# Optimization experiments

Hardware: AMD Instinct MI355X
Metric: run time of the kernel (lower is better)

## Reference

```python
import jax, jax.numpy as jnp
import numpy as np

NEG_SLOPE = 0.2  # PyG GATv2Conv default negative_slope
G = 128          # number of graphs in the batch


def _gatv2(x, src, dst, n, Wl, bl, Wr, br, att, bias, H, C):
    # x: [N, in]; src/dst: [E] (self-loops already appended)
    xl = (x @ Wl + bl).reshape(n, H, C)   # lin_l -> used for source nodes
    xr = (x @ Wr + br).reshape(n, H, C)   # lin_r -> used for target nodes
    e = jax.nn.leaky_relu(xl[src] + xr[dst], NEG_SLOPE)      # [E,H,C]
    logit = jnp.einsum('ehc,hc->eh', e, att)                 # [E,H]
    # softmax over edges grouped by destination node
    m = jax.ops.segment_max(logit, dst, num_segments=n)      # [N,H]
    p = jnp.exp(logit - m[dst])
    denom = jax.ops.segment_sum(p, dst, num_segments=n)
    alpha = p / denom[dst]                                   # [E,H]
    out = jax.ops.segment_sum(xl[src] * alpha[..., None], dst, num_segments=n)
    return out.reshape(n, H * C) + bias                      # concat heads + bias


def setup_inputs() -> dict:
    key = jax.random.key(0)
    ks = jax.random.split(key, 32)
    N, E, V, EMB = 30000, 480000, 10000, 16
    s = 0.1
    d = {
        'emb':  jax.random.normal(ks[0], (V, EMB)) * s,
        'Wl0':  jax.random.normal(ks[1], (16, 96)) * s,
        'bl0':  jax.random.normal(ks[2], (96,)) * s,
        'Wr0':  jax.random.normal(ks[3], (16, 96)) * s,
        'br0':  jax.random.normal(ks[4], (96,)) * s,
        'att0': jax.random.normal(ks[5], (3, 32)) * s,
        'bo0':  jax.random.normal(ks[6], (96,)) * s,
        'Wl1':  jax.random.normal(ks[7], (96, 192)) * s,
        'bl1':  jax.random.normal(ks[8], (192,)) * s,
        'Wr1':  jax.random.normal(ks[9], (96, 192)) * s,
        'br1':  jax.random.normal(ks[10], (192,)) * s,
        'att1': jax.random.normal(ks[11], (2, 96)) * s,
        'bo1':  jax.random.normal(ks[12], (192,)) * s,
        'Wl2':  jax.random.normal(ks[13], (192, 64)) * s,
        'bl2':  jax.random.normal(ks[14], (64,)) * s,
        'Wr2':  jax.random.normal(ks[15], (192, 64)) * s,
        'br2':  jax.random.normal(ks[16], (64,)) * s,
        'att2': jax.random.normal(ks[17], (1, 64)) * s,
        'bo2':  jax.random.normal(ks[18], (64,)) * s,
        'Wc1':  jax.random.normal(ks[19], (69, 32)) * s,
        'bc1':  jax.random.normal(ks[20], (32,)) * s,
        'Wc2':  jax.random.normal(ks[21], (32, 2)) * s,
        'bc2':  jax.random.normal(ks[22], (2,)) * s,
        'demographics': jax.random.normal(ks[23], (G, 5)),
        'node_ids': jax.random.randint(ks[24], (N,), 0, V),
        'edge_index': jax.random.randint(ks[25], (2, E), 0, N),
        'batch': jnp.sort(jax.random.randint(ks[26], (N,), 0, G)),
    }
    return d


def reference(emb, Wl0, bl0, Wr0, br0, att0, bo0,
              Wl1, bl1, Wr1, br1, att1, bo1,
              Wl2, bl2, Wr2, br2, att2, bo2,
              Wc1, bc1, Wc2, bc2, demographics,
              node_ids, edge_index, batch):
    N = node_ids.shape[0]
    x = emb[node_ids]                                  # node embedding lookup
    loops = jnp.arange(N)
    src = jnp.concatenate([edge_index[0], loops])      # PyG add_self_loops=True
    dst = jnp.concatenate([edge_index[1], loops])
    x = _gatv2(x, src, dst, N, Wl0, bl0, Wr0, br0, att0, bo0, 3, 32)
    x = _gatv2(x, src, dst, N, Wl1, bl1, Wr1, br1, att1, bo1, 2, 96)
    x = _gatv2(x, src, dst, N, Wl2, bl2, Wr2, br2, att2, bo2, 1, 64)
    # global mean pool over graphs
    counts = jax.ops.segment_sum(jnp.ones((N,), x.dtype), batch, num_segments=G)
    g = jax.ops.segment_sum(x, batch, num_segments=G) / jnp.maximum(counts, 1.0)[:, None]
    h = jnp.concatenate([g, demographics], axis=1)     # [G, 64+5]
    h = jax.nn.relu(h @ Wc1 + bc1)                     # dropout is identity at eval
    return h @ Wc2 + bc2                               # out_dim=2 -> no squeeze
```

## Files before the change

kernel.cpp:

```cpp
#include <hip/hip_runtime.h>
#include <hip/hip_bf16.h>

typedef __hip_bfloat16 bf16;
typedef __attribute__((ext_vector_type(8))) short short8;
typedef __attribute__((ext_vector_type(4))) float f32x4;

static __device__ __forceinline__ float b2f(bf16 v){ return __bfloat162float(v); }
static __device__ __forceinline__ float blo(unsigned u){ return __uint_as_float(u<<16); }
static __device__ __forceinline__ float bhi(unsigned u){ return __uint_as_float(u & 0xffff0000u); }
static __device__ __forceinline__ int clampi(int v, int lo, int hi){
  return v < lo ? lo : (v > hi ? hi : v);
}
static __device__ __forceinline__ unsigned pack2(float lo, float hi){
  bf16 a = __float2bfloat16(lo), b = __float2bfloat16(hi);
  unsigned short ua, ub;
  __builtin_memcpy(&ua,&a,2); __builtin_memcpy(&ub,&b,2);
  return (unsigned)ua | ((unsigned)ub<<16);
}
static __device__ __forceinline__ float fexp2(float x){ return __builtin_exp2f(x); }

template<int CTRL>
static __device__ __forceinline__ float dppadd(float v){
  int s = __builtin_amdgcn_update_dpp(0, __float_as_int(v), CTRL, 0xf, 0xf, false);
  return v + __int_as_float(s);
}
static __device__ __forceinline__ float red16(float v){
  v = dppadd<0x121>(v);
  v = dppadd<0x122>(v);
  v = dppadd<0x124>(v);
  v = dppadd<0x128>(v);
  return v;
}

constexpr int Nn = 30000;
constexpr int E0 = 480000;
constexpr int EP = E0 + Nn;
constexpr int Gg = 128;
constexpr int Vv = 10000;
constexpr int CAP = 64;
constexpr float L2E = 1.4426950408889634f;

__global__ void k_flag(float* __restrict__ out, float v){
  int t = blockIdx.x*blockDim.x + threadIdx.x;
  if (t < Gg*2) out[t] = v;
}

__global__ void k_prep(const float* __restrict__ emb, const int* __restrict__ ids,
                       bf16* __restrict__ x, int* __restrict__ cursor,
                       const float* __restrict__ W0l, const float* __restrict__ W0r,
                       const float* __restrict__ W1l, const float* __restrict__ W1r,
                       const float* __restrict__ W2l, const float* __restrict__ W2r,
                       bf16* __restrict__ B0l, bf16* __restrict__ B0r,
                       bf16* __restrict__ B1l, bf16* __restrict__ B1r,
                       bf16* __restrict__ B2l, bf16* __restrict__ B2r){
  int t = blockIdx.x*blockDim.x + threadIdx.x;
  if (t < Nn) cursor[t] = 0;
  if (t < 67584){
    const float* W; bf16* B; int K, F, KS, i;
    if      (t <  3072){ i = t;       W = W0l; B = B0l; K=16;  F=96;  KS=1; }
    else if (t <  6144){ i = t-3072;  W = W0r; B = B0r; K=16;  F=96;  KS=1; }
    else if (t < 24576){ i = t-6144;  W = W1l; B = B1l; K=96;  F=192; KS=3; }
    else if (t < 43008){ i = t-24576; W = W1r; B = B1r; K=96;  F=192; KS=3; }
    else if (t < 55296){ i = t-43008; W = W2l; B = B2l; K=192; F=64;  KS=6; }
    else               { i = t-55296; W = W2r; B = B2r; K=192; F=64;  KS=6; }
    int f = i >> 3, j = i & 7;
    int ot   = f / (KS*64);
    int rem  = f % (KS*64);
    int ks   = rem >> 6;
    int lane = rem & 63;
    int l16  = lane & 15, quad = lane >> 4;
    int o = ot*16 + l16;
    int k = ks*32 + quad*8 + j;
    float v = (k < K) ? W[k*F + o] : 0.f;
    B[i] = __float2bfloat16(v);
  }
  if (t < Nn*16){
    int n = t >> 4, c = t & 15;
    int id = clampi(ids[n], 0, Vv-1);
    x[t] = __float2bfloat16(emb[id*16 + c]);
  }
}

template<int K, int Kp, int Fout>
static __device__ __forceinline__
void linB_body(int bid, const bf16* __restrict__ x,
               const bf16* __restrict__ Wbl, const float* __restrict__ bl,
               const bf16* __restrict__ Wbr, const float* __restrict__ br,
               bf16* __restrict__ yl, bf16* __restrict__ yr){
  constexpr int OT = Fout/16, KS = Kp/32;
  constexpr int FR = OT*KS*64;
  __shared__ uint4 sB[FR];
  constexpr int MT = Nn/16;
  int wid = threadIdx.x >> 6, lane = threadIdx.x & 63;
  int grp = bid*4 + wid;
  int l16 = lane & 15, quad = lane >> 4;
  bool havework = (grp < MT);

  short8 a[KS];
  if (havework){
    const bf16* arow = x + (size_t)(grp*16 + l16)*K;
    #pragma unroll
    for (int ks=0; ks<KS; ks++){
      int k0 = ks*32 + quad*8;
      if (K == Kp || k0 < K) a[ks] = *(const short8*)(arow + k0);
      else                   a[ks] = short8{0,0,0,0,0,0,0,0};
    }
  }
  #pragma unroll
  for (int side=0; side<2; side++){
    const bf16*  Wb   = side ? Wbr : Wbl;
    const float* bias = side ? br  : bl;
    bf16*        y    = side ? yr  : yl;
    const uint4* srcp = (const uint4*)Wb;
    for (int idx = threadIdx.x; idx < FR; idx += 256) sB[idx] = srcp[idx];
    __syncthreads();
    if (havework){
      #pragma unroll
      for (int ot=0; ot<OT; ot++){
        f32x4 acc = {0.f,0.f,0.f,0.f};
        #pragma unroll
        for (int ks=0; ks<KS; ks++){
          short8 b = *(const short8*)&sB[(ot*KS + ks)*64 + lane];
          acc = __builtin_amdgcn_mfma_f32_16x16x32_bf16(a[ks], b, acc, 0, 0, 0);
        }
        int o0 = ot*16;
        float bo_ = bias[o0 + l16];
        #pragma unroll
        for (int r=0;r<4;r++){
          int m = grp*16 + quad*4 + r;
          y[(size_t)m*Fout + o0 + l16] = __float2bfloat16(acc[r] + bo_);
        }
      }
    }
    __syncthreads();
  }
}

template<int K, int Kp, int Fout>
__global__ __launch_bounds__(256) void k_linB(const bf16* __restrict__ x,
               const bf16* __restrict__ Wbl, const float* __restrict__ bl,
               const bf16* __restrict__ Wbr, const float* __restrict__ br,
               bf16* __restrict__ yl, bf16* __restrict__ yr){
  linB_body<K,Kp,Fout>(blockIdx.x, x, Wbl, bl, Wbr, br, yl, yr);
}

constexpr int CBcnt = (EP + 255) / 256;
__global__ __launch_bounds__(256) void k_fillin0(const int* __restrict__ ei,
               int* __restrict__ cursor, int* __restrict__ bucket,
               const bf16* __restrict__ x,
               const bf16* __restrict__ Wbl, const float* __restrict__ bl,
               const bf16* __restrict__ Wbr, const float* __restrict__ br,
               bf16* __restrict__ yl, bf16* __restrict__ yr){
  if ((int)blockIdx.x < CBcnt){
    int e = blockIdx.x*256 + threadIdx.x;
    if (e < EP){
      int src = (e < E0) ? clampi(ei[e],      0, Nn-1) : (e - E0);
      int dst = (e < E0) ? clampi(ei[E0 + e], 0, Nn-1) : (e - E0);
      int pos = atomicAdd(&cursor[dst], 1);
      if (pos < CAP) bucket[dst*CAP + pos] = src;
    }
    return;
  }
  linB_body<16,32,96>(blockIdx.x - CBcnt, x, Wbl, bl, Wbr, br, yl, yr);
}


template<int UN, bool MASK>
static __device__ __forceinline__
void idx0(const int* __restrict__ eb, int i, int r1, int g, unsigned off[UN]){
  #pragma unroll
  for (int u=0;u<UN;u++){
    int iu = i + 4*u + g;
    int ii = MASK ? ((iu<r1)? iu : (r1-1)) : iu;
    off[u] = (unsigned)eb[ii] * 96u;
  }
}

template<int UN, bool MASK>
static __device__ __forceinline__
void body0(const bf16* __restrict__ xl0, const unsigned off[UN],
           int i, int r1, int g,
           const float xr2[3][2], const float a06[3][2], const float a04[3][2],
           float acc[3][2], float ds[3]){
  unsigned xw[UN][3];
  #pragma unroll
  for (int u=0;u<UN;u++){
    xw[u][0] = *(const unsigned*)(xl0 + off[u]);
    xw[u][1] = *(const unsigned*)(xl0 + off[u] + 32);
    xw[u][2] = *(const unsigned*)(xl0 + off[u] + 64);
  }
  #pragma unroll
  for (int u=0;u<UN;u++){
    float wm = MASK ? (((i + 4*u + g) < r1) ? 1.f : 0.f) : 1.f;
    #pragma unroll
    for (int h=0;h<3;h++){
      float c0 = blo(xw[u][h]), c1 = bhi(xw[u][h]);
      float z0 = c0 + xr2[h][0], z1 = c1 + xr2[h][1];
      float ts = a06[h][0]*z0;
      ts = fmaf(a04[h][0], __builtin_fabsf(z0), ts);
      ts = fmaf(a06[h][1], z1, ts);
      ts = fmaf(a04[h][1], __builtin_fabsf(z1), ts);
      float hs = red16(ts);
      float p = fexp2(hs);
      if (MASK) p *= wm;
      acc[h][0] += p*c0; acc[h][1] += p*c1; ds[h] += p;
    }
  }
}

__global__ void k_fused0w(const bf16* __restrict__ xl, const bf16* __restrict__ xr,
                          const int* __restrict__ bucket, const int* __restrict__ cursor,
                          const float* __restrict__ att, const float* __restrict__ bo,
                          bf16* __restrict__ y){
  int n = blockIdx.x*(blockDim.x>>6) + (threadIdx.x>>6);
  if (n >= Nn) return;
  int lane = threadIdx.x & 63;
  int g = lane >> 4, l16 = lane & 15, c2 = 2*l16;
  const bf16* xl0 = xl + c2;
  const int* eb = bucket + n*CAP;
  int r1 = cursor[n]; if (r1 > CAP) r1 = CAP;
  float xr2[3][2], a06[3][2], a04[3][2];
  #pragma unroll
  for (int h=0;h<3;h++){
    unsigned wv = *(const unsigned*)(xr + (size_t)n*96 + h*32 + c2);
    xr2[h][0]=blo(wv); xr2[h][1]=bhi(wv);
    float2 av = *(const float2*)(att + h*32 + c2);
    a06[h][0]=0.6f*L2E*av.x; a04[h][0]=0.4f*L2E*av.x;
    a06[h][1]=0.6f*L2E*av.y; a04[h][1]=0.4f*L2E*av.y;
  }
  float acc[3][2] = {{0.f,0.f},{0.f,0.f},{0.f,0.f}};
  float ds[3] = {0.f,0.f,0.f};
  int i = 0;
  int nw = r1 >> 4;
  if (nw > 0){
    unsigned offA[4], offB[4];
    idx0<4,false>(eb, i, r1, g, offA);
    for (int k=0; k<nw-1; k++){
      idx0<4,false>(eb, i+16, r1, g, offB);
      body0<4,false>(xl0, offA, i, r1, g, xr2, a06, a04, acc, ds);
      #pragma unroll
      for (int u=0;u<4;u++) offA[u] = offB[u];
      i += 16;
    }
    body0<4,false>(xl0, offA, i, r1, g, xr2, a06, a04, acc, ds);
    i += 16;
  }
  int rem = r1 - i;
  if (rem > 0){
    unsigned offT[4];
    if (rem > 8){
      idx0<4,true>(eb, i, r1, g, offT);
      body0<4,true>(xl0, offT, i, r1, g, xr2, a06, a04, acc, ds);
    } else if (rem > 4){
      idx0<2,true>(eb, i, r1, g, offT);
      body0<2,true>(xl0, offT, i, r1, g, xr2, a06, a04, acc, ds);
    } else {
      idx0<1,true>(eb, i, r1, g, offT);
      body0<1,true>(xl0, offT, i, r1, g, xr2, a06, a04, acc, ds);
    }
  }
  #pragma unroll
  for (int h=0;h<3;h++){
    #pragma unroll
    for (int j=0;j<2;j++){
      acc[h][j] += __shfl_xor(acc[h][j],16,64);
      acc[h][j] += __shfl_xor(acc[h][j],32,64);
    }
    ds[h] += __shfl_xor(ds[h],16,64);
    ds[h] += __shfl_xor(ds[h],32,64);
  }
  if (g == 0){
    #pragma unroll
    for (int h=0;h<3;h++){
      float inv = 1.f/fmaxf(ds[h],1e-30f);
      unsigned pw = pack2(acc[h][0]*inv + bo[h*32+c2], acc[h][1]*inv + bo[h*32+c2+1]);
      *(unsigned*)(y + (size_t)n*96 + h*32 + c2) = pw;
    }
  }
}

template<int UN, bool MASK>
static __device__ __forceinline__
void idx1(const int* __restrict__ eb, int i, int r1, int esel, unsigned off[UN]){
  #pragma unroll
  for (int u=0;u<UN;u++){
    int iu = i + 2*u + esel;
    int ii = MASK ? ((iu<r1)? iu : (r1-1)) : iu;
    off[u] = (unsigned)eb[ii] * 192u;
  }
}

template<int UN, bool MASK>
static __device__ __forceinline__
void body1(const bf16* __restrict__ xlA, const bf16* __restrict__ xlB,
           const unsigned off[UN], int i, int r1, int esel,
           const float xr6[6], const float a06[6], const float a04[6],
           float acc[6], float& ds){
  uint2 xa[UN]; unsigned xb[UN];
  #pragma unroll
  for (int u=0;u<UN;u++){
    xa[u] = *(const uint2*)(xlA + off[u]);
    xb[u] = *(const unsigned*)(xlB + off[u]);
  }
  #pragma unroll
  for (int u=0;u<UN;u++){
    float wm = MASK ? (((i + 2*u + esel) < r1) ? 1.f : 0.f) : 1.f;
    float c[6];
    c[0]=blo(xa[u].x); c[1]=bhi(xa[u].x);
    c[2]=blo(xa[u].y); c[3]=bhi(xa[u].y);
    c[4]=blo(xb[u]);   c[5]=bhi(xb[u]);
    float ts = 0.f;
    #pragma unroll
    for (int j=0;j<6;j++){
      float z = c[j] + xr6[j];
      ts = fmaf(a06[j], z, ts);
      ts = fmaf(a04[j], __builtin_fabsf(z), ts);
    }
    float hs = red16(ts);
    float p = fexp2(hs);
    if (MASK) p *= wm;
    #pragma unroll
    for (int j=0;j<6;j++) acc[j] += p*c[j];
    ds += p;
  }
}

__global__ void k_fused1w(const bf16* __restrict__ xl, const bf16* __restrict__ xr,
                          const int* __restrict__ bucket, const int* __restrict__ cursor,
                          const float* __restrict__ att, const float* __restrict__ bo,
                          bf16* __restrict__ y){
  int n = blockIdx.x*(blockDim.x>>6) + (threadIdx.x>>6);
  if (n >= Nn) return;
  int lane = threadIdx.x & 63;
  int l16 = lane & 15;
  int head = (lane >> 4) & 1;
  int esel = lane >> 5;
  int chA = head*96 + 4*l16;
  int chB = head*96 + 64 + 2*l16;
  const bf16* xlA = xl + chA;
  const bf16* xlB = xl + chB;
  const int* eb = bucket + n*CAP;
  int r1 = cursor[n]; if (r1 > CAP) r1 = CAP;
  uint2 xra = *(const uint2*)(xr + (size_t)n*192 + chA);
  unsigned xrb = *(const unsigned*)(xr + (size_t)n*192 + chB);
  float xr6[6] = { blo(xra.x), bhi(xra.x), blo(xra.y), bhi(xra.y), blo(xrb), bhi(xrb) };
  float4 aA = *(const float4*)(att + chA);
  float2 aB = *(const float2*)(att + chB);
  float a06[6] = {0.6f*L2E*aA.x,0.6f*L2E*aA.y,0.6f*L2E*aA.z,0.6f*L2E*aA.w,0.6f*L2E*aB.x,0.6f*L2E*aB.y};
  float a04[6] = {0.4f*L2E*aA.x,0.4f*L2E*aA.y,0.4f*L2E*aA.z,0.4f*L2E*aA.w,0.4f*L2E*aB.x,0.4f*L2E*aB.y};
  float acc[6] = {0.f,0.f,0.f,0.f,0.f,0.f};
  float ds = 0.f;
  int i = 0;
  int nw = r1 >> 4;
  if (nw > 0){
    unsigned offA[8], offB[8];
    idx1<8,false>(eb, i, r1, esel, offA);
    for (int k=0; k<nw-1; k++){
      idx1<8,false>(eb, i+16, r1, esel, offB);
      body1<8,false>(xlA, xlB, offA, i, r1, esel, xr6, a06, a04, acc, ds);
      #pragma unroll
      for (int u=0;u<8;u++) offA[u] = offB[u];
      i += 16;
    }
    body1<8,false>(xlA, xlB, offA, i, r1, esel, xr6, a06, a04, acc, ds);
    i += 16;
  }
  int rem = r1 - i;
  if (rem > 0){
    unsigned offT[8];
    if (rem > 8){
      idx1<8,true>(eb, i, r1, esel, offT);
      body1<8,true>(xlA, xlB, offT, i, r1, esel, xr6, a06, a04, acc, ds);
    } else if (rem > 4){
      idx1<4,true>(eb, i, r1, esel, offT);
      body1<4,true>(xlA, xlB, offT, i, r1, esel, xr6, a06, a04, acc, ds);
    } else if (rem > 2){
      idx1<2,true>(eb, i, r1, esel, offT);
      body1<2,true>(xlA, xlB, offT, i, r1, esel, xr6, a06, a04, acc, ds);
    } else {
      idx1<1,true>(eb, i, r1, esel, offT);
      body1<1,true>(xlA, xlB, offT, i, r1, esel, xr6, a06, a04, acc, ds);
    }
  }
  #pragma unroll
  for (int j=0;j<6;j++) acc[j] += __shfl_xor(acc[j],32,64);
  ds += __shfl_xor(ds,32,64);
  if (esel == 0){
    float inv = 1.f/fmaxf(ds,1e-30f);
    unsigned p0 = pack2(acc[0]*inv + bo[chA  ], acc[1]*inv + bo[chA+1]);
    unsigned p1 = pack2(acc[2]*inv + bo[chA+2], acc[3]*inv + bo[chA+3]);
    unsigned p2 = pack2(acc[4]*inv + bo[chB  ], acc[5]*inv + bo[chB+1]);
    *(unsigned*)(y + (size_t)n*192 + chA    ) = p0;
    *(unsigned*)(y + (size_t)n*192 + chA + 2) = p1;
    *(unsigned*)(y + (size_t)n*192 + chB    ) = p2;
  }
}

template<int UN, bool MASK>
static __device__ __forceinline__
void idx2(const int* __restrict__ eb, int i, int r1, int g, unsigned off[UN]){
  #pragma unroll
  for (int u=0;u<UN;u++){
    int iu = i + 4*u + g;
    int ii = MASK ? ((iu<r1)? iu : (r1-1)) : iu;
    off[u] = (unsigned)eb[ii] * 64u;
  }
}

template<int UN, bool MASK>
static __device__ __forceinline__
void body2(const bf16* __restrict__ xl2, const unsigned off[UN],
           int i, int r1, int g,
           const float xr4[4], const float a06[4], const float a04[4],
           float acc[4], float& ds){
  uint2 xw[UN];
  #pragma unroll
  for (int u=0;u<UN;u++) xw[u] = *(const uint2*)(xl2 + off[u]);
  #pragma unroll
  for (int u=0;u<UN;u++){
    float wm = MASK ? (((i + 4*u + g) < r1) ? 1.f : 0.f) : 1.f;
    float c[4];
    c[0]=blo(xw[u].x); c[1]=bhi(xw[u].x);
    c[2]=blo(xw[u].y); c[3]=bhi(xw[u].y);
    float ts = 0.f;
    #pragma unroll
    for (int j=0;j<4;j++){
      float z = c[j] + xr4[j];
      ts = fmaf(a06[j], z, ts);
      ts = fmaf(a04[j], __builtin_fabsf(z), ts);
    }
    float hs = red16(ts);
    float p = fexp2(hs);
    if (MASK) p *= wm;
    #pragma unroll
    for (int j=0;j<4;j++) acc[j] += p*c[j];
    ds += p;
  }
}

__global__ void k_fused2w(const bf16* __restrict__ xl, const bf16* __restrict__ xr,
                          const int* __restrict__ bucket, const int* __restrict__ cursor,
                          const float* __restrict__ att, const float* __restrict__ bo,
                          bf16* __restrict__ y){
  int n = blockIdx.x*(blockDim.x>>6) + (threadIdx.x>>6);
  if (n >= Nn) return;
  int lane = threadIdx.x & 63;
  int g = lane >> 4, l16 = lane & 15;
  int ch = 4*l16;
  const bf16* xl2 = xl + ch;
  const int* eb = bucket + n*CAP;
  int r1 = cursor[n]; if (r1 > CAP) r1 = CAP;
  uint2 xrw = *(const uint2*)(xr + (size_t)n*64 + ch);
  float xr4[4] = { blo(xrw.x), bhi(xrw.x), blo(xrw.y), bhi(xrw.y) };
  float4 a4 = *(const float4*)(att + ch);
  float a06[4] = {0.6f*L2E*a4.x,0.6f*L2E*a4.y,0.6f*L2E*a4.z,0.6f*L2E*a4.w};
  float a04[4] = {0.4f*L2E*a4.x,0.4f*L2E*a4.y,0.4f*L2E*a4.z,0.4f*L2E*a4.w};
  float acc[4] = {0.f,0.f,0.f,0.f};
  float ds = 0.f;
  int i = 0;
  int nw = r1 >> 4;
  if (nw > 0){
    unsigned offA[4], offB[4];
    idx2<4,false>(eb, i, r1, g, offA);
    for (int k=0; k<nw-1; k++){
      idx2<4,false>(eb, i+16, r1, g, offB);
      body2<4,false>(xl2, offA, i, r1, g, xr4, a06, a04, acc, ds);
      #pragma unroll
      for (int u=0;u<4;u++) offA[u] = offB[u];
      i += 16;
    }
    body2<4,false>(xl2, offA, i, r1, g, xr4, a06, a04, acc, ds);
    i += 16;
  }
  int rem = r1 - i;
  if (rem > 0){
    unsigned offT[4];
    if (rem > 8){
      idx2<4,true>(eb, i, r1, g, offT);
      body2<4,true>(xl2, offT, i, r1, g, xr4, a06, a04, acc, ds);
    } else if (rem > 4){
      idx2<2,true>(eb, i, r1, g, offT);
      body2<2,true>(xl2, offT, i, r1, g, xr4, a06, a04, acc, ds);
    } else {
      idx2<1,true>(eb, i, r1, g, offT);
      body2<1,true>(xl2, offT, i, r1, g, xr4, a06, a04, acc, ds);
    }
  }
  #pragma unroll
  for (int j=0;j<4;j++){
    acc[j] += __shfl_xor(acc[j],16,64);
    acc[j] += __shfl_xor(acc[j],32,64);
  }
  ds += __shfl_xor(ds,16,64);
  ds += __shfl_xor(ds,32,64);
  if (g == 0){
    float inv = 1.f/fmaxf(ds,1e-30f);
    unsigned p0 = pack2(acc[0]*inv + bo[ch  ], acc[1]*inv + bo[ch+1]);
    unsigned p1 = pack2(acc[2]*inv + bo[ch+2], acc[3]*inv + bo[ch+3]);
    uint2 pw; pw.x = p0; pw.y = p1;
    *(uint2*)(y + (size_t)n*64 + ch) = pw;
  }
}

__global__ void k_poolhead(const bf16* __restrict__ x, const int* __restrict__ batch,
                           const float* __restrict__ demo,
                           const float* __restrict__ Wc1, const float* __restrict__ bc1,
                           const float* __restrict__ Wc2, const float* __restrict__ bc2,
                           float* __restrict__ out){
  __shared__ float sh[4][64];
  __shared__ float h0[69];
  __shared__ float h1[32];
  int g = blockIdx.x;
  int t = threadIdx.x;
  int c = t & 63;
  int w = t >> 6;
  int a = 0, b = Nn;
  while (a < b){ int m = (a+b)>>1; if (clampi(batch[m],0,Gg-1) < g) a = m+1; else b = m; }
  int lo = a;
  b = Nn;
  while (a < b){ int m = (a+b)>>1; if (clampi(batch[m],0,Gg-1) <= g) a = m+1; else b = m; }
  int hi = a;

  float s = 0.f;
  for (int n = lo + w; n < hi; n += 4)
    s += b2f(x[(size_t)n*64 + c]);
  sh[w][c] = s;
  __syncthreads();
  float invc = 1.f / fmaxf((float)(hi - lo), 1.f);
  if (t < 64) h0[t] = (sh[0][t] + sh[1][t] + sh[2][t] + sh[3][t]) * invc;
  else if (t < 69) h0[t] = demo[g*5 + (t - 64)];
  __syncthreads();
  if (t < 32){
    float v = bc1[t];
    for (int k=0;k<69;k++) v += h0[k]*Wc1[k*32 + t];
    h1[t] = fmaxf(v, 0.f);
  }
  __syncthreads();
  if (t < 2){
    float v = bc2[t];
    for (int k=0;k<32;k++) v += h1[k]*Wc2[k*2 + t];
    out[g*2 + t] = v;
  }
}

extern "C" void kernel_launch(void* const* d_in, const int* in_sizes, int n_in,
                              void* d_out, int out_size, void* d_ws, size_t ws_size,
                              hipStream_t stream) {
  const float* emb  = (const float*)d_in[0];
  const float* Wl0  = (const float*)d_in[1];
  const float* bl0  = (const float*)d_in[2];
  const float* Wr0  = (const float*)d_in[3];
  const float* br0  = (const float*)d_in[4];
  const float* att0 = (const float*)d_in[5];
  const float* bo0  = (const float*)d_in[6];
  const float* Wl1  = (const float*)d_in[7];
  const float* bl1  = (const float*)d_in[8];
  const float* Wr1  = (const float*)d_in[9];
  const float* br1  = (const float*)d_in[10];
  const float* att1 = (const float*)d_in[11];
  const float* bo1  = (const float*)d_in[12];
  const float* Wl2  = (const float*)d_in[13];
  const float* bl2  = (const float*)d_in[14];
  const float* Wr2  = (const float*)d_in[15];
  const float* br2  = (const float*)d_in[16];
  const float* att2 = (const float*)d_in[17];
  const float* bo2  = (const float*)d_in[18];
  const float* Wc1  = (const float*)d_in[19];
  const float* bc1  = (const float*)d_in[20];
  const float* Wc2  = (const float*)d_in[21];
  const float* bc2  = (const float*)d_in[22];
  const float* demo = (const float*)d_in[23];
  const int* node_ids = (const int*)d_in[24];
  const int* ei       = (const int*)d_in[25];
  const int* batch    = (const int*)d_in[26];
  float* out = (float*)d_out;

  bool ok = (n_in == 27) && (out_size == Gg*2)
         && (in_sizes[0]  == Vv*16) && (in_sizes[1]  == 16*96)
         && (in_sizes[7]  == 96*192) && (in_sizes[13] == 192*64)
         && (in_sizes[19] == 69*32) && (in_sizes[23] == Gg*5)
         && (in_sizes[24] == Nn) && (in_sizes[25] == 2*E0) && (in_sizes[26] == Nn);
  if (!ok){ k_flag<<<1, 256, 0, stream>>>(out, 4000.f); return; }

  size_t need = 0;
  auto plan = [&](size_t bytes){ size_t r = need; need += (bytes + 255) & ~(size_t)255; return r; };
  size_t o_x      = plan((size_t)Nn*192*2);
  size_t o_xl     = plan((size_t)Nn*192*2);
  size_t o_xr     = plan((size_t)Nn*192*2);
  size_t o_cursor = plan((size_t)Nn*4);
  size_t o_bucket = plan((size_t)Nn*CAP*4);
  size_t o_wb0l   = plan((size_t)96*32*2);
  size_t o_wb0r   = plan((size_t)96*32*2);
  size_t o_wb1l   = plan((size_t)192*96*2);
  size_t o_wb1r   = plan((size_t)192*96*2);
  size_t o_wb2l   = plan((size_t)64*192*2);
  size_t o_wb2r   = plan((size_t)64*192*2);
  if (need > ws_size){ k_flag<<<1, 256, 0, stream>>>(out, 5000.f); return; }

  char* p = (char*)d_ws;
  bf16*  x      = (bf16*) (p + o_x);
  bf16*  xl     = (bf16*) (p + o_xl);
  bf16*  xr     = (bf16*) (p + o_xr);
  int*   cursor = (int*)  (p + o_cursor);
  int*   bucket = (int*)  (p + o_bucket);
  bf16*  wb0l   = (bf16*) (p + o_wb0l);
  bf16*  wb0r   = (bf16*) (p + o_wb0r);
  bf16*  wb1l   = (bf16*) (p + o_wb1l);
  bf16*  wb1r   = (bf16*) (p + o_wb1r);
  bf16*  wb2l   = (bf16*) (p + o_wb2l);
  bf16*  wb2r   = (bf16*) (p + o_wb2r);

  k_prep<<<(Nn*16+255)/256, 256, 0, stream>>>(emb, node_ids, x, cursor,
                                              Wl0, Wr0, Wl1, Wr1, Wl2, Wr2,
                                              wb0l, wb0r, wb1l, wb1r, wb2l, wb2r);

  constexpr int MT = Nn/16;
  constexpr int LB = (MT+3)/4;
  int wgrid = (Nn+3)/4;

  k_fillin0<<<CBcnt + LB, 256, 0, stream>>>(ei, cursor, bucket, x,
                                            wb0l, bl0, wb0r, br0, xl, xr);

  k_fused0w<<<wgrid, 256, 0, stream>>>(xl, xr, bucket, cursor, att0, bo0, x);

  k_linB<96,96,192><<<LB, 256, 0, stream>>>(x, wb1l, bl1, wb1r, br1, xl, xr);
  k_fused1w<<<wgrid, 256, 0, stream>>>(xl, xr, bucket, cursor, att1, bo1, x);

  k_linB<192,192,64><<<LB, 256, 0, stream>>>(x, wb2l, bl2, wb2r, br2, xl, xr);
  k_fused2w<<<wgrid, 256, 0, stream>>>(xl, xr, bucket, cursor, att2, bo2, x);

  k_poolhead<<<Gg, 256, 0, stream>>>(x, batch, demo, Wc1, bc1, Wc2, bc2, out);
}
```

Before: 277.7 us.

## Pad cursor counters, pre-seed self-loops, and batch two edges per thread in fill

Each per-node atomic cursor now sits on its own 64-byte stride to cut contention and false sharing between neighbouring destinations. Self-loop edges are written into the bucket during prep, with the cursor starting at 1, so the fill kernel only handles real edges. Each fill thread now processes two edges and issues both atomics before the stores, and the linear-layer blocks are placed first in the combined grid so they start earlier. The cost is a 16x larger cursor array and sparser reads of the cursor in the fused kernels.

New measurement: 257.7 us. -7.2%, faster.

```diff
diff --git a/kernel.cpp b/kernel.cpp
--- a/kernel.cpp
+++ b/kernel.cpp
@@ -38,6 +38,7 @@
 constexpr int Gg = 128;
 constexpr int Vv = 10000;
 constexpr int CAP = 64;
+constexpr int CPAD = 16;
 constexpr float L2E = 1.4426950408889634f;
 
 __global__ void k_flag(float* __restrict__ out, float v){
@@ -46,7 +47,7 @@
 }
 
 __global__ void k_prep(const float* __restrict__ emb, const int* __restrict__ ids,
-                       bf16* __restrict__ x, int* __restrict__ cursor,
+                       bf16* __restrict__ x, int* __restrict__ cursor, int* __restrict__ bucket,
                        const float* __restrict__ W0l, const float* __restrict__ W0r,
                        const float* __restrict__ W1l, const float* __restrict__ W1r,
                        const float* __restrict__ W2l, const float* __restrict__ W2r,
@@ -54,7 +55,7 @@
                        bf16* __restrict__ B1l, bf16* __restrict__ B1r,
                        bf16* __restrict__ B2l, bf16* __restrict__ B2r){
   int t = blockIdx.x*blockDim.x + threadIdx.x;
-  if (t < Nn) cursor[t] = 0;
+  if (t < Nn){ cursor[t*CPAD] = 1; bucket[t*CAP] = t; }
   if (t < 67584){
     const float* W; bf16* B; int K, F, KS, i;
     if      (t <  3072){ i = t;       W = W0l; B = B0l; K=16;  F=96;  KS=1; }
@@ -144,24 +145,31 @@
   linB_body<K,Kp,Fout>(blockIdx.x, x, Wbl, bl, Wbr, br, yl, yr);
 }
 
-constexpr int CBcnt = (EP + 255) / 256;
+constexpr int MTc = Nn/16;
+constexpr int LB  = (MTc+3)/4;
+constexpr int FBf = (E0/2 + 255)/256;
 __global__ __launch_bounds__(256) void k_fillin0(const int* __restrict__ ei,
                int* __restrict__ cursor, int* __restrict__ bucket,
                const bf16* __restrict__ x,
                const bf16* __restrict__ Wbl, const float* __restrict__ bl,
                const bf16* __restrict__ Wbr, const float* __restrict__ br,
                bf16* __restrict__ yl, bf16* __restrict__ yr){
-  if ((int)blockIdx.x < CBcnt){
-    int e = blockIdx.x*256 + threadIdx.x;
-    if (e < EP){
-      int src = (e < E0) ? clampi(ei[e],      0, Nn-1) : (e - E0);
-      int dst = (e < E0) ? clampi(ei[E0 + e], 0, Nn-1) : (e - E0);
-      int pos = atomicAdd(&cursor[dst], 1);
-      if (pos < CAP) bucket[dst*CAP + pos] = src;
-    }
+  if ((int)blockIdx.x < LB){
+    linB_body<16,32,96>(blockIdx.x, x, Wbl, bl, Wbr, br, yl, yr);
     return;
   }
-  linB_body<16,32,96>(blockIdx.x - CBcnt, x, Wbl, bl, Wbr, br, yl, yr);
+  int b = blockIdx.x - LB;
+  int e0 = b*512 + threadIdx.x;
+  int e1 = e0 + 256;
+  bool v0 = e0 < E0, v1 = e1 < E0;
+  int src0=0, dst0=0, src1=0, dst1=0;
+  if (v0){ src0 = clampi(ei[e0],0,Nn-1); dst0 = clampi(ei[E0+e0],0,Nn-1); }
+  if (v1){ src1 = clampi(ei[e1],0,Nn-1); dst1 = clampi(ei[E0+e1],0,Nn-1); }
+  int p0=0, p1=0;
+  if (v0) p0 = atomicAdd(&cursor[dst0*CPAD], 1);
+  if (v1) p1 = atomicAdd(&cursor[dst1*CPAD], 1);
+  if (v0 && p0 < CAP) bucket[dst0*CAP + p0] = src0;
+  if (v1 && p1 < CAP) bucket[dst1*CAP + p1] = src1;
 }
 
 
@@ -218,7 +226,7 @@
   int g = lane >> 4, l16 = lane & 15, c2 = 2*l16;
   const bf16* xl0 = xl + c2;
   const int* eb = bucket + n*CAP;
-  int r1 = cursor[n]; if (r1 > CAP) r1 = CAP;
+  int r1 = cursor[n*CPAD]; if (r1 > CAP) r1 = CAP;
   float xr2[3][2], a06[3][2], a04[3][2];
   #pragma unroll
   for (int h=0;h<3;h++){
@@ -340,7 +348,7 @@
   const bf16* xlA = xl + chA;
   const bf16* xlB = xl + chB;
   const int* eb = bucket + n*CAP;
-  int r1 = cursor[n]; if (r1 > CAP) r1 = CAP;
+  int r1 = cursor[n*CPAD]; if (r1 > CAP) r1 = CAP;
   uint2 xra = *(const uint2*)(xr + (size_t)n*192 + chA);
   unsigned xrb = *(const unsigned*)(xr + (size_t)n*192 + chB);
   float xr6[6] = { blo(xra.x), bhi(xra.x), blo(xra.y), bhi(xra.y), blo(xrb), bhi(xrb) };
@@ -449,7 +457,7 @@
   int ch = 4*l16;
   const bf16* xl2 = xl + ch;
   const int* eb = bucket + n*CAP;
-  int r1 = cursor[n]; if (r1 > CAP) r1 = CAP;
+  int r1 = cursor[n*CPAD]; if (r1 > CAP) r1 = CAP;
   uint2 xrw = *(const uint2*)(xr + (size_t)n*64 + ch);
   float xr4[4] = { blo(xrw.x), bhi(xrw.x), blo(xrw.y), bhi(xrw.y) };
   float4 a4 = *(const float4*)(att + ch);
@@ -587,7 +595,7 @@
   size_t o_x      = plan((size_t)Nn*192*2);
   size_t o_xl     = plan((size_t)Nn*192*2);
   size_t o_xr     = plan((size_t)Nn*192*2);
-  size_t o_cursor = plan((size_t)Nn*4);
+  size_t o_cursor = plan((size_t)Nn*CPAD*4);
   size_t o_bucket = plan((size_t)Nn*CAP*4);
   size_t o_wb0l   = plan((size_t)96*32*2);
   size_t o_wb0r   = plan((size_t)96*32*2);
@@ -610,16 +618,14 @@
   bf16*  wb2l   = (bf16*) (p + o_wb2l);
   bf16*  wb2r   = (bf16*) (p + o_wb2r);
 
-  k_prep<<<(Nn*16+255)/256, 256, 0, stream>>>(emb, node_ids, x, cursor,
+  k_prep<<<(Nn*16+255)/256, 256, 0, stream>>>(emb, node_ids, x, cursor, bucket,
                                               Wl0, Wr0, Wl1, Wr1, Wl2, Wr2,
                                               wb0l, wb0r, wb1l, wb1r, wb2l, wb2r);
 
-  constexpr int MT = Nn/16;
-  constexpr int LB = (MT+3)/4;
   int wgrid = (Nn+3)/4;
 
-  k_fillin0<<<CBcnt + LB, 256, 0, stream>>>(ei, cursor, bucket, x,
-                                            wb0l, bl0, wb0r, br0, xl, xr);
+  k_fillin0<<<LB + FBf, 256, 0, stream>>>(ei, cursor, bucket, x,
+                                          wb0l, bl0, wb0r, br0, xl, xr);
 
   k_fused0w<<<wgrid, 256, 0, stream>>>(xl, xr, bucket, cursor, att0, bo0, x);
 
```
